# Kernel tuning notes

Measured on AMD Instinct MI355X. Metric: run time of the kernel, lower is better.

Reference implementation:

```python
import jax, jax.numpy as jnp
import numpy as np

B = 64          # number of graphs (batch_size)
NPG = 400       # nodes per graph (>= left_nodes)
K = 250         # left_nodes (TopKPooling ratio as int)
F = 64          # feat_dim
S = 12          # seq_len
LIN = K * F     # 16000, flattened pooled features
H = LIN // 2    # 8000, hidden dim of MLP
EPS = 1e-5      # BatchNorm eps


def setup_inputs() -> dict:
    key = jax.random.key(0)
    ks = jax.random.split(key, 10)
    N = B * NPG
    features = jax.random.normal(ks[0], (S, N, F), jnp.float32)
    edge_index = jax.random.randint(ks[1], (2, N * 16), 0, N, dtype=jnp.int64)
    batch = (jnp.arange(N) // NPG).astype(jnp.int64)  # sorted graph ids, 400 nodes each
    # TopKPooling learnable score vector
    w = jax.random.normal(ks[2], (F,), jnp.float32) * 0.1
    # BatchNorm1d (eval mode) parameters / running stats
    bn_gamma = jax.random.uniform(ks[3], (LIN,), jnp.float32, 0.5, 1.5)
    bn_beta = jax.random.normal(ks[4], (LIN,), jnp.float32) * 0.1
    bn_mean = jax.random.normal(ks[5], (LIN,), jnp.float32) * 0.1
    bn_var = jax.random.uniform(ks[6], (LIN,), jnp.float32, 0.5, 1.5)
    # MLP: Linear(LIN, LIN//2) -> ReLU -> Linear(LIN//2, 1)
    W1 = jax.random.normal(ks[7], (H, LIN), jnp.float32) * (1.0 / np.sqrt(LIN))
    b1 = jnp.zeros((H,), jnp.float32)
    W2 = jax.random.normal(ks[8], (1, H), jnp.float32) * (1.0 / np.sqrt(H))
    b2 = jnp.zeros((1,), jnp.float32)
    return {"features": features, "edge_index": edge_index, "batch": batch,
            "w": w, "bn_gamma": bn_gamma, "bn_beta": bn_beta,
            "bn_mean": bn_mean, "bn_var": bn_var,
            "W1": W1, "b1": b1, "W2": W2, "b2": b2}


def reference(features, edge_index, batch, w, bn_gamma, bn_beta, bn_mean, bn_var, W1, b1, W2, b2):
    # Last timestep only, as in forward(): x_ = features[-1, ...]
    x = features[-1]                                   # [N, F]
    # PyG TopKPooling: score = (x @ w) / ||w||, select top-k per graph,
    # rescale selected nodes by tanh(score).
    score = (x @ w) / jnp.linalg.norm(w)               # [N]
    sb = score.reshape(B, NPG)                         # graphs are contiguous
    vals, idx = jax.lax.top_k(sb, K)                   # [B, K], descending per graph
    xb = x.reshape(B, NPG, F)
    sel = jnp.take_along_axis(xb, idx[:, :, None], axis=1) * jnp.tanh(vals)[:, :, None]
    flat = sel.reshape(B, LIN)                         # x_.view(batch_size, -1)
    # BatchNorm1d in eval mode (running stats); dropout is identity in eval.
    xn = (flat - bn_mean) / jnp.sqrt(bn_var + EPS) * bn_gamma + bn_beta
    h = jax.nn.relu(xn @ W1.T + b1)                    # [B, H]
    logits = (h @ W2.T + b2).astype(jnp.float32)       # [B, 1]
    # city != tgt -> batch_truth = ones; BCEWithLogits(x, y) = softplus(x) - x*y
    truth = jnp.ones((B, 1), jnp.float32)
    loss = jnp.mean(jax.nn.softplus(logits) - logits * truth)
    return loss
```

## Files before the change

kernel.cpp:

```cpp
#include <hip/hip_runtime.h>
#include <hip/hip_bf16.h>
#include <math.h>

#define NGRAPH 64
#define NPG_   400
#define KSEL   250
#define FDIM   64
#define SEQ    12
#define LIN_   16000
#define HDIM   8000
#define NTOT   (NGRAPH*NPG_)
#define BN_EPS 1e-5f
#define JBLK   32
#define NBLK   (HDIM/JBLK)

typedef float          floatx4  __attribute__((ext_vector_type(4)));
typedef unsigned int   uintx4   __attribute__((ext_vector_type(4)));
typedef unsigned short ushortx8 __attribute__((ext_vector_type(8)));
typedef __bf16         bf16x8   __attribute__((ext_vector_type(8)));

__device__ inline unsigned short f2bf(float x) {
    unsigned u = __float_as_uint(x);
    u += 0x7FFFu + ((u >> 16) & 1u);
    return (unsigned short)(u >> 16);
}

__global__ __launch_bounds__(256) void pool_bn_kernel(
    const float* __restrict__ features, const float* __restrict__ w,
    const float* __restrict__ gamma, const float* __restrict__ beta,
    const float* __restrict__ mean, const float* __restrict__ var,
    unsigned short* __restrict__ xnA)
{
    __shared__ float s_w[FDIM];
    __shared__ float s_rnorm;
    __shared__ float s_score[NPG_];
    __shared__ int   s_idx[KSEL];
    __shared__ float s_scale[KSEL];

    const int g = blockIdx.x;
    const int t = threadIdx.x;
    const float* __restrict__ x = features + (size_t)(SEQ - 1) * NTOT * FDIM;

    if (t < FDIM) s_w[t] = w[t];
    __syncthreads();
    if (t == 0) {
        float s = 0.f;
        #pragma unroll
        for (int i = 0; i < FDIM; ++i) s += s_w[i] * s_w[i];
        s_rnorm = 1.0f / sqrtf(s);
    }
    __syncthreads();
    const float rnorm = s_rnorm;

    for (int i = t; i < NPG_; i += 256) {
        const floatx4* xr = (const floatx4*)(x + (size_t)(g * NPG_ + i) * FDIM);
        float s = 0.f;
        #pragma unroll
        for (int q = 0; q < FDIM / 4; ++q) {
            floatx4 v = xr[q];
            s += v[0]*s_w[4*q] + v[1]*s_w[4*q+1] + v[2]*s_w[4*q+2] + v[3]*s_w[4*q+3];
        }
        s_score[i] = s * rnorm;
    }
    __syncthreads();

    for (int i = t; i < NPG_; i += 256) {
        const float si = s_score[i];
        int r = 0;
        for (int jj = 0; jj < NPG_; ++jj) {
            const float sj = s_score[jj];
            r += (sj > si) || (sj == si && jj < i);
        }
        if (r < KSEL) { s_idx[r] = i; s_scale[r] = tanhf(si); }
    }
    __syncthreads();

    const size_t rowbase = (size_t)g * LIN_;
    for (int c = t; c < LIN_; c += 256) {
        const int p = c >> 6, f = c & 63;
        const int node = g * NPG_ + s_idx[p];
        const float v = x[(size_t)node * FDIM + f] * s_scale[p];
        const float xnv = (v - mean[c]) * rsqrtf(var[c] + BN_EPS) * gamma[c] + beta[c];
        xnA[rowbase + c] = f2bf(xnv);
    }
}

__global__ __launch_bounds__(256) void gemm_kernel(
    const float* __restrict__ W1, const unsigned short* __restrict__ xnA,
    const float* __restrict__ b1, const float* __restrict__ W2,
    float* __restrict__ partials)
{
    const int t = threadIdx.x;
    const int wave = t >> 6, lane = t & 63;
    const int jt = wave >> 1, par = wave & 1;
    const int blk = blockIdx.x;
    const int n = lane & 15, kg = lane >> 4;
    const int j = blk * JBLK + jt * 16 + n;

    const size_t boff  = (size_t)j * LIN_ + kg * 8;
    const size_t aoff0 = (size_t)(n)      * LIN_ + kg * 8;
    const size_t aoff1 = aoff0 + (size_t)16 * LIN_;
    const size_t aoff2 = aoff1 + (size_t)16 * LIN_;
    const size_t aoff3 = aoff2 + (size_t)16 * LIN_;

    floatx4 acc0 = {0,0,0,0}, acc1 = {0,0,0,0}, acc2 = {0,0,0,0}, acc3 = {0,0,0,0};

    int k = par * 32;
    floatx4 pb0 = *(const floatx4*)(W1 + boff + k);
    floatx4 pb1 = *(const floatx4*)(W1 + boff + k + 4);
    uintx4  pa0 = *(const uintx4*)(xnA + aoff0 + k);
    uintx4  pa1 = *(const uintx4*)(xnA + aoff1 + k);
    uintx4  pa2 = *(const uintx4*)(xnA + aoff2 + k);
    uintx4  pa3 = *(const uintx4*)(xnA + aoff3 + k);

    for (int s = 0; s < 250; ++s) {
        const int kn = k + 64;
        const int kl = (s < 249) ? kn : par * 32;
        floatx4 nb0 = *(const floatx4*)(W1 + boff + kl);
        floatx4 nb1 = *(const floatx4*)(W1 + boff + kl + 4);
        uintx4  na0 = *(const uintx4*)(xnA + aoff0 + kl);
        uintx4  na1 = *(const uintx4*)(xnA + aoff1 + kl);
        uintx4  na2 = *(const uintx4*)(xnA + aoff2 + kl);
        uintx4  na3 = *(const uintx4*)(xnA + aoff3 + kl);

        ushortx8 bs;
        bs[0] = f2bf(pb0[0]); bs[1] = f2bf(pb0[1]); bs[2] = f2bf(pb0[2]); bs[3] = f2bf(pb0[3]);
        bs[4] = f2bf(pb1[0]); bs[5] = f2bf(pb1[1]); bs[6] = f2bf(pb1[2]); bs[7] = f2bf(pb1[3]);
        const bf16x8 bfrag = __builtin_bit_cast(bf16x8, bs);

        acc0 = __builtin_amdgcn_mfma_f32_16x16x32_bf16(__builtin_bit_cast(bf16x8, pa0), bfrag, acc0, 0, 0, 0);
        acc1 = __builtin_amdgcn_mfma_f32_16x16x32_bf16(__builtin_bit_cast(bf16x8, pa1), bfrag, acc1, 0, 0, 0);
        acc2 = __builtin_amdgcn_mfma_f32_16x16x32_bf16(__builtin_bit_cast(bf16x8, pa2), bfrag, acc2, 0, 0, 0);
        acc3 = __builtin_amdgcn_mfma_f32_16x16x32_bf16(__builtin_bit_cast(bf16x8, pa3), bfrag, acc3, 0, 0, 0);

        pb0 = nb0; pb1 = nb1;
        pa0 = na0; pa1 = na1; pa2 = na2; pa3 = na3;
        k = kn;
    }

    __shared__ float hbuf[64][33];
    const int col  = jt * 16 + n;
    const int mrow = kg * 4;
    if (par == 0) {
        #pragma unroll
        for (int r = 0; r < 4; ++r) {
            hbuf[ 0 + mrow + r][col] = acc0[r];
            hbuf[16 + mrow + r][col] = acc1[r];
            hbuf[32 + mrow + r][col] = acc2[r];
            hbuf[48 + mrow + r][col] = acc3[r];
        }
    }
    __syncthreads();
    if (par == 1) {
        #pragma unroll
        for (int r = 0; r < 4; ++r) {
            hbuf[ 0 + mrow + r][col] += acc0[r];
            hbuf[16 + mrow + r][col] += acc1[r];
            hbuf[32 + mrow + r][col] += acc2[r];
            hbuf[48 + mrow + r][col] += acc3[r];
        }
    }
    __syncthreads();

    const int m = t >> 2, jq = t & 3;
    float s = 0.f;
    #pragma unroll
    for (int q = 0; q < 8; ++q) {
        const int jj = jq * 8 + q;
        float h = hbuf[m][jj] + b1[blk * JBLK + jj];
        h = fmaxf(h, 0.f);
        s += h * W2[blk * JBLK + jj];
    }
    s += __shfl_xor(s, 1);
    s += __shfl_xor(s, 2);
    if (jq == 0) partials[blk * 64 + m] = s;
}

__global__ __launch_bounds__(64) void loss_kernel(
    const float* __restrict__ partials, const float* __restrict__ b2,
    float* __restrict__ out)
{
    const int b = threadIdx.x;
    float l = b2[0];
    for (int i = 0; i < NBLK; ++i) l += partials[i * 64 + b];
    float ls = fmaxf(-l, 0.f) + log1pf(expf(-fabsf(l)));
    #pragma unroll
    for (int d = 1; d < 64; d <<= 1) ls += __shfl_xor(ls, d);
    if (b == 0) out[0] = ls * (1.0f / 64.0f);
}

extern "C" void kernel_launch(void* const* d_in, const int* in_sizes, int n_in,
                              void* d_out, int out_size, void* d_ws, size_t ws_size,
                              hipStream_t stream)
{
    const float* features = (const float*)d_in[0];
    const float* w     = (const float*)d_in[3];
    const float* gamma = (const float*)d_in[4];
    const float* beta  = (const float*)d_in[5];
    const float* mean  = (const float*)d_in[6];
    const float* var   = (const float*)d_in[7];
    const float* W1    = (const float*)d_in[8];
    const float* b1    = (const float*)d_in[9];
    const float* W2    = (const float*)d_in[10];
    const float* b2    = (const float*)d_in[11];

    unsigned short* xnA = (unsigned short*)d_ws;
    float* partials = (float*)((char*)d_ws + 2048000);

    pool_bn_kernel<<<NGRAPH, 256, 0, stream>>>(features, w, gamma, beta, mean, var, xnA);
    gemm_kernel<<<NBLK, 256, 0, stream>>>(W1, xnA, b1, W2, partials);
    loss_kernel<<<1, 64, 0, stream>>>(partials, b2, (float*)d_out);
}
```

Baseline: 840.5 us.

## Split GEMM K-loop across four waves and double-buffer global loads

The GEMM block grows from 256 to 512 threads, so each 16-column tile is now reduced over K by four waves instead of two, each wave striding 128 elements. The K loop is unrolled by two with two register sets of W1 and activation loads in flight, giving a deeper prefetch. The aim is more outstanding memory requests per CU to hide latency on the fp32 W1 stream. In exchange, register pressure rises under the launch_bounds(512,2) hint, and the partial sums are combined through four serialized shared-memory passes with extra barriers.

```diff
diff --git a/kernel.cpp b/kernel.cpp
--- a/kernel.cpp
+++ b/kernel.cpp
@@ -85,14 +85,14 @@
     }
 }
 
-__global__ __launch_bounds__(256) void gemm_kernel(
+__global__ __launch_bounds__(512, 2) void gemm_kernel(
     const float* __restrict__ W1, const unsigned short* __restrict__ xnA,
     const float* __restrict__ b1, const float* __restrict__ W2,
     float* __restrict__ partials)
 {
     const int t = threadIdx.x;
     const int wave = t >> 6, lane = t & 63;
-    const int jt = wave >> 1, par = wave & 1;
+    const int jt = wave >> 2, par = wave & 3;
     const int blk = blockIdx.x;
     const int n = lane & 15, kg = lane >> 4;
     const int j = blk * JBLK + jt * 16 + n;
@@ -105,74 +105,83 @@
 
     floatx4 acc0 = {0,0,0,0}, acc1 = {0,0,0,0}, acc2 = {0,0,0,0}, acc3 = {0,0,0,0};
 
-    int k = par * 32;
-    floatx4 pb0 = *(const floatx4*)(W1 + boff + k);
-    floatx4 pb1 = *(const floatx4*)(W1 + boff + k + 4);
-    uintx4  pa0 = *(const uintx4*)(xnA + aoff0 + k);
-    uintx4  pa1 = *(const uintx4*)(xnA + aoff1 + k);
-    uintx4  pa2 = *(const uintx4*)(xnA + aoff2 + k);
-    uintx4  pa3 = *(const uintx4*)(xnA + aoff3 + k);
-
-    for (int s = 0; s < 250; ++s) {
-        const int kn = k + 64;
-        const int kl = (s < 249) ? kn : par * 32;
-        floatx4 nb0 = *(const floatx4*)(W1 + boff + kl);
-        floatx4 nb1 = *(const floatx4*)(W1 + boff + kl + 4);
-        uintx4  na0 = *(const uintx4*)(xnA + aoff0 + kl);
-        uintx4  na1 = *(const uintx4*)(xnA + aoff1 + kl);
-        uintx4  na2 = *(const uintx4*)(xnA + aoff2 + kl);
-        uintx4  na3 = *(const uintx4*)(xnA + aoff3 + kl);
-
-        ushortx8 bs;
-        bs[0] = f2bf(pb0[0]); bs[1] = f2bf(pb0[1]); bs[2] = f2bf(pb0[2]); bs[3] = f2bf(pb0[3]);
-        bs[4] = f2bf(pb1[0]); bs[5] = f2bf(pb1[1]); bs[6] = f2bf(pb1[2]); bs[7] = f2bf(pb1[3]);
-        const bf16x8 bfrag = __builtin_bit_cast(bf16x8, bs);
-
-        acc0 = __builtin_amdgcn_mfma_f32_16x16x32_bf16(__builtin_bit_cast(bf16x8, pa0), bfrag, acc0, 0, 0, 0);
-        acc1 = __builtin_amdgcn_mfma_f32_16x16x32_bf16(__builtin_bit_cast(bf16x8, pa1), bfrag, acc1, 0, 0, 0);
-        acc2 = __builtin_amdgcn_mfma_f32_16x16x32_bf16(__builtin_bit_cast(bf16x8, pa2), bfrag, acc2, 0, 0, 0);
-        acc3 = __builtin_amdgcn_mfma_f32_16x16x32_bf16(__builtin_bit_cast(bf16x8, pa3), bfrag, acc3, 0, 0, 0);
-
-        pb0 = nb0; pb1 = nb1;
-        pa0 = na0; pa1 = na1; pa2 = na2; pa3 = na3;
-        k = kn;
-    }
+#define LOAD_SET(PB0,PB1,PA0,PA1,PA2,PA3,KK) do {            \
+        PB0 = *(const floatx4*)(W1 + boff + (KK));           \
+        PB1 = *(const floatx4*)(W1 + boff + (KK) + 4);       \
+        PA0 = *(const uintx4*)(xnA + aoff0 + (KK));          \
+        PA1 = *(const uintx4*)(xnA + aoff1 + (KK));          \
+        PA2 = *(const uintx4*)(xnA + aoff2 + (KK));          \
+        PA3 = *(const uintx4*)(xnA + aoff3 + (KK));          \
+    } while (0)
+
+#define CVT_MFMA(PB0,PB1,PA0,PA1,PA2,PA3) do {                                  \
+        ushortx8 bs;                                                            \
+        bs[0]=f2bf(PB0[0]); bs[1]=f2bf(PB0[1]); bs[2]=f2bf(PB0[2]); bs[3]=f2bf(PB0[3]); \
+        bs[4]=f2bf(PB1[0]); bs[5]=f2bf(PB1[1]); bs[6]=f2bf(PB1[2]); bs[7]=f2bf(PB1[3]); \
+        const bf16x8 bfrag = __builtin_bit_cast(bf16x8, bs);                    \
+        acc0 = __builtin_amdgcn_mfma_f32_16x16x32_bf16(__builtin_bit_cast(bf16x8, PA0), bfrag, acc0, 0, 0, 0); \
+        acc1 = __builtin_amdgcn_mfma_f32_16x16x32_bf16(__builtin_bit_cast(bf16x8, PA1), bfrag, acc1, 0, 0, 0); \
+        acc2 = __builtin_amdgcn_mfma_f32_16x16x32_bf16(__builtin_bit_cast(bf16x8, PA2), bfrag, acc2, 0, 0, 0); \
+        acc3 = __builtin_amdgcn_mfma_f32_16x16x32_bf16(__builtin_bit_cast(bf16x8, PA3), bfrag, acc3, 0, 0, 0); \
+    } while (0)
+
+    const int k00 = par * 32;
+    floatx4 pb0, pb1; uintx4 pa0, pa1, pa2, pa3;
+    floatx4 qb0, qb1; uintx4 qa0, qa1, qa2, qa3;
+
+    LOAD_SET(pb0,pb1,pa0,pa1,pa2,pa3, k00);
+    LOAD_SET(qb0,qb1,qa0,qa1,qa2,qa3, k00 + 128);
+
+    int k = k00;
+    for (int it = 0; it < 62; ++it) {
+        CVT_MFMA(pb0,pb1,pa0,pa1,pa2,pa3);
+        LOAD_SET(pb0,pb1,pa0,pa1,pa2,pa3, k + 256);
+        CVT_MFMA(qb0,qb1,qa0,qa1,qa2,qa3);
+        const int kl = (it < 61) ? (k + 384) : k00;
+        LOAD_SET(qb0,qb1,qa0,qa1,qa2,qa3, kl);
+        k += 256;
+    }
+    CVT_MFMA(pb0,pb1,pa0,pa1,pa2,pa3);
+
+#undef LOAD_SET
+#undef CVT_MFMA
 
     __shared__ float hbuf[64][33];
     const int col  = jt * 16 + n;
     const int mrow = kg * 4;
-    if (par == 0) {
-        #pragma unroll
-        for (int r = 0; r < 4; ++r) {
-            hbuf[ 0 + mrow + r][col] = acc0[r];
-            hbuf[16 + mrow + r][col] = acc1[r];
-            hbuf[32 + mrow + r][col] = acc2[r];
-            hbuf[48 + mrow + r][col] = acc3[r];
+    #pragma unroll
+    for (int p = 0; p < 4; ++p) {
+        if (par == p) {
+            #pragma unroll
+            for (int r = 0; r < 4; ++r) {
+                if (p == 0) {
+                    hbuf[ 0 + mrow + r][col] = acc0[r];
+                    hbuf[16 + mrow + r][col] = acc1[r];
+                    hbuf[32 + mrow + r][col] = acc2[r];
+                    hbuf[48 + mrow + r][col] = acc3[r];
+                } else {
+                    hbuf[ 0 + mrow + r][col] += acc0[r];
+                    hbuf[16 + mrow + r][col] += acc1[r];
+                    hbuf[32 + mrow + r][col] += acc2[r];
+                    hbuf[48 + mrow + r][col] += acc3[r];
+                }
+            }
         }
-    }
-    __syncthreads();
-    if (par == 1) {
-        #pragma unroll
-        for (int r = 0; r < 4; ++r) {
-            hbuf[ 0 + mrow + r][col] += acc0[r];
-            hbuf[16 + mrow + r][col] += acc1[r];
-            hbuf[32 + mrow + r][col] += acc2[r];
-            hbuf[48 + mrow + r][col] += acc3[r];
-        }
-    }
-    __syncthreads();
-
-    const int m = t >> 2, jq = t & 3;
+        __syncthreads();
+    }
+
+    const int m = t >> 3, jq = t & 7;
     float s = 0.f;
     #pragma unroll
-    for (int q = 0; q < 8; ++q) {
-        const int jj = jq * 8 + q;
+    for (int q = 0; q < 4; ++q) {
+        const int jj = jq * 4 + q;
         float h = hbuf[m][jj] + b1[blk * JBLK + jj];
         h = fmaxf(h, 0.f);
         s += h * W2[blk * JBLK + jj];
     }
     s += __shfl_xor(s, 1);
     s += __shfl_xor(s, 2);
+    s += __shfl_xor(s, 4);
     if (jq == 0) partials[blk * 64 + m] = s;
 }
 
@@ -208,6 +217,6 @@
     float* partials = (float*)((char*)d_ws + 2048000);
 
     pool_bn_kernel<<<NGRAPH, 256, 0, stream>>>(features, w, gamma, beta, mean, var, xnA);
-    gemm_kernel<<<NBLK, 256, 0, stream>>>(W1, xnA, b1, W2, partials);
+    gemm_kernel<<<NBLK, 512, 0, stream>>>(W1, xnA, b1, W2, partials);
     loss_kernel<<<1, 64, 0, stream>>>(partials, b2, (float*)d_out);
 }
```

Result: no change. 847.3 us (+0.8%).
